# Kernel optimization log

Hardware: AMD Instinct MI355X
Metric: run time of the kernel (lower is better)

## Reference

```python
import jax, jax.numpy as jnp
import numpy as np

B = 2            # graphs per batch
N_SRC = 4096     # src nodes per graph
N_TGT = 4096     # tgt nodes per graph
NX = 8; NY = 8   # subdomain grid
C_IN = 8; HID = 32; C_OUT = 8
ENC = 2 * HID    # input_encode output dim, matches GraphConv(2*hidden, out)


def _clusters(coords, batch):
    cx = np.clip((coords[:, 0] * NX).astype(np.int64), 0, NX - 1)
    cy = np.clip((coords[:, 1] * NY).astype(np.int64), 0, NY - 1)
    return batch * (NX * NY) + cx * NY + cy


def setup_inputs() -> dict:
    rng = np.random.default_rng(0)
    src_coords = rng.random((B * N_SRC, 2)).astype(np.float32)
    tgt_coords = rng.random((B * N_TGT, 2)).astype(np.float32)
    src_batch = np.repeat(np.arange(B), N_SRC).astype(np.int32)
    tgt_batch = np.repeat(np.arange(B), N_TGT).astype(np.int32)
    # subdomain clustering + all-pairs intra-cluster edges, self loops removed
    sub = np.concatenate([_clusters(src_coords, src_batch.astype(np.int64)),
                          _clusters(tgt_coords, tgt_batch.astype(np.int64))])
    rows, cols = [], []
    for c in range(B * NX * NY):
        idx = np.nonzero(sub == c)[0]
        a, b = np.meshgrid(idx, idx, indexing='ij')
        m = a != b
        rows.append(a[m]); cols.append(b[m])
    edge_index = np.stack([np.concatenate(rows), np.concatenate(cols)]).astype(np.int32)

    def lin(k, fan_in, fan_out):
        return (rng.standard_normal((fan_in, fan_out)).astype(np.float32) / np.sqrt(fan_in))

    return {
        'src_node_values': jnp.asarray(rng.standard_normal((B * N_SRC, C_IN)).astype(np.float32)),
        'src_coords': jnp.asarray(src_coords),
        'src_batch': jnp.asarray(src_batch),
        'tgt_node_values': jnp.asarray(rng.standard_normal((B * N_TGT, C_IN)).astype(np.float32)),
        'tgt_coords': jnp.asarray(tgt_coords),
        'tgt_batch': jnp.asarray(tgt_batch),
        'edge_index': jnp.asarray(edge_index),
        'W_enc': jnp.asarray(lin(0, C_IN + 2, ENC)),
        'b_enc': jnp.zeros((ENC,), jnp.float32),
        'W_skip': jnp.asarray(lin(1, C_IN, C_OUT)),
        'W_rel': jnp.asarray(lin(2, ENC, C_OUT)),
        'b_rel': jnp.zeros((C_OUT,), jnp.float32),
        'W_root': jnp.asarray(lin(3, ENC, C_OUT)),
    }


def reference(src_node_values, src_coords, src_batch, tgt_node_values, tgt_coords,
              tgt_batch, edge_index, W_enc, b_enc, W_skip, W_rel, b_rel, W_root):
    pos = jnp.concatenate([src_coords, tgt_coords], axis=0)            # [N,2]
    vals = jnp.concatenate([src_node_values, tgt_node_values], axis=0)  # [N,Cin]
    x = jnp.concatenate([vals, pos], axis=1) @ W_enc + b_enc           # [N,2H]
    N = x.shape[0]
    src_j, dst_i = edge_index[0], edge_index[1]
    # edge_weight = ||pos_i - pos_j|| (self loops already removed)
    w = jnp.linalg.norm(pos[src_j] - pos[dst_i], axis=1)               # [E]
    msg = w[:, None] * x[src_j]                                        # [E,2H]
    agg = jax.ops.segment_sum(msg, dst_i, num_segments=N)
    cnt = jax.ops.segment_sum(jnp.ones_like(w), dst_i, num_segments=N)
    agg = agg / jnp.maximum(cnt, 1.0)[:, None]                         # mean aggr
    out = agg @ W_rel + b_rel + x @ W_root                             # GraphConv
    return tgt_node_values @ W_skip + out[src_coords.shape[0]:]
```

## Files before the change

### kernel.cpp

```cpp
#include <hip/hip_runtime.h>
#include <math.h>

#define NSRC 8192
#define NC   128
#define MAXN 256
#define MAXT 128
#define QT   32
#define KPAD 260

__device__ inline void fma4(float4& a, float s, const float4 w) {
    a.x = fmaf(s, w.x, a.x); a.y = fmaf(s, w.y, a.y);
    a.z = fmaf(s, w.z, a.z); a.w = fmaf(s, w.w, a.w);
}

__global__ __launch_bounds__(256) void fused_kernel(
        const float* __restrict__ sv, const float* __restrict__ sc,
        const float* __restrict__ tv, const float* __restrict__ tc,
        const float* __restrict__ W_enc, const float* __restrict__ b_enc,
        const float* __restrict__ W_skip, const float* __restrict__ W_rel,
        const float* __restrict__ b_rel, const float* __restrict__ W_root,
        float* __restrict__ out) {
    __shared__ float mpx[MAXN], mpy[MAXN];
    __shared__ int   mids[MAXN];
    __shared__ int   rslot[MAXN];
    __shared__ int   tIdx[MAXT];
    __shared__ int   wsum[4];
    __shared__ float Wer[10][8];
    __shared__ float Woz[10][8];
    __shared__ float c01[16];
    __shared__ float yL[MAXN][8];
    __shared__ float zL[QT][8];
    __shared__ float tpxB[QT], tpyB[QT];
    __shared__ int   tmidB[QT];
    __shared__ float2 pL[QT][4][2];
    __shared__ float wL[QT][KPAD];

    const int c = blockIdx.x >> 2, quarter = blockIdx.x & 3;
    const int t = threadIdx.x;
    const int lane = t & 63, wid = t >> 6;
    const float4* scp = (const float4*)sc;
    const float4* tcp = (const float4*)tc;

    rslot[t] = -1;

    unsigned long long mask = 0ull;
    int cnt = 0, cntT = 0;
#pragma unroll 8
    for (int i = 0; i < 32; ++i) {
        int idx4 = i * 256 + t;
        int isT = idx4 >= 4096;
        float4 qd = isT ? tcp[idx4 - 4096] : scp[idx4];
        int local0 = (idx4 - (isT ? 4096 : 0)) * 2;
        int b = local0 >> 12;
        int cx0 = min(max((int)(qd.x * 8.0f), 0), 7);
        int cy0 = min(max((int)(qd.y * 8.0f), 0), 7);
        int cx1 = min(max((int)(qd.z * 8.0f), 0), 7);
        int cy1 = min(max((int)(qd.w * 8.0f), 0), 7);
        if (b * 64 + cx0 * 8 + cy0 == c) { mask |= 1ull << (2 * i);     cnt++; cntT += isT; }
        if (b * 64 + cx1 * 8 + cy1 == c) { mask |= 1ull << (2 * i + 1); cnt++; cntT += isT; }
    }
    int incl = cnt | (cntT << 16);
    for (int s = 1; s < 64; s <<= 1) {
        int v = __shfl_up(incl, s, 64);
        if (lane >= s) incl += v;
    }
    if (lane == 63) wsum[wid] = incl;
    __syncthreads();
    int pre = 0, total = 0;
    for (int w = 0; w < 4; ++w) { int v = wsum[w]; if (w < wid) pre += v; total += v; }
    incl += pre;
    const int ncl_total = total & 0xffff;
    const int ncl = min(ncl_total, MAXN);
    const int ntT = min(total >> 16, MAXT);
    const int clen = (ntT + 3) >> 2;
    const int qlo = quarter * clen;
    const int myNT = min(clen, ntT - qlo);
    if (myNT <= 0) return;
    int p = (incl & 0xffff) - cnt;
    int q = (incl >> 16) - cntT;

    int bpos[8];
#pragma unroll
    for (int j = 0; j < 8; ++j) {
        bpos[j] = mask ? (__ffsll((unsigned long long)mask) - 1) : -1;
        mask &= mask - 1;
    }
#pragma unroll
    for (int j = 0; j < 8; ++j) {
        if (bpos[j] >= 0) {
            int i = bpos[j] >> 1, jj = bpos[j] & 1;
            int idx4 = i * 256 + t;
            int isT = idx4 >= 4096;
            float4 q4 = isT ? tcp[idx4 - 4096] : scp[idx4];
            float px = jj ? q4.z : q4.x, py = jj ? q4.w : q4.y;
            int nl = (idx4 - (isT ? 4096 : 0)) * 2 + jj;
            if (p < MAXN) {
                mids[p] = isT ? (NSRC + nl) : nl;
                mpx[p] = px; mpy[p] = py;
                if (isT && q < MAXT) { tIdx[q] = p; rslot[p] = q; }
            }
            p++; if (isT) q++;
        }
    }
    while (mask) {
        int bp = __ffsll((unsigned long long)mask) - 1;
        mask &= mask - 1;
        int i = bp >> 1, jj = bp & 1;
        int idx4 = i * 256 + t;
        int isT = idx4 >= 4096;
        float4 q4 = isT ? tcp[idx4 - 4096] : scp[idx4];
        int nl = (idx4 - (isT ? 4096 : 0)) * 2 + jj;
        if (p < MAXN) {
            mids[p] = isT ? (NSRC + nl) : nl;
            mpx[p] = jj ? q4.z : q4.x; mpy[p] = jj ? q4.w : q4.y;
            if (isT && q < MAXT) { tIdx[q] = p; rslot[p] = q; }
        }
        p++; if (isT) q++;
    }

    if (t < 176) {
        const float* ap; const float* bp2; float init; float* dst;
        if (t < 80) {
            int r = t >> 3, o = t & 7;
            ap = W_enc + r * 64; bp2 = W_rel + o; init = 0.f; dst = &Wer[r][o];
        } else if (t < 160) {
            int u = t - 80, r = u >> 3, o = u & 7;
            ap = W_enc + r * 64; bp2 = W_root + o;
            init = (r < 8) ? W_skip[r * 8 + o] : 0.f; dst = &Woz[r][o];
        } else if (t < 168) {
            int o = t - 160;
            ap = b_enc; bp2 = W_rel + o; init = 0.f; dst = &c01[o];
        } else {
            int o = t - 168;
            ap = b_enc; bp2 = W_root + o; init = b_rel[o]; dst = &c01[8 + o];
        }
        float acc = init;
#pragma unroll 8
        for (int h = 0; h < 64; ++h) acc = fmaf(ap[h], bp2[h * 8], acc);
        *dst = acc;
    }
    __syncthreads();

    if (t < ncl) {
        const int gid = mids[t];
        const float* vals = (gid < NSRC) ? (sv + gid * 8) : (tv + (gid - NSRC) * 8);
        const float4 v0 = *(const float4*)vals;
        const float4 v1 = *(const float4*)(vals + 4);
        const float px = mpx[t], py = mpy[t];
        float4 y0 = *(const float4*)&c01[0];
        float4 y1 = *(const float4*)&c01[4];
        fma4(y0, v0.x, *(const float4*)&Wer[0][0]); fma4(y1, v0.x, *(const float4*)&Wer[0][4]);
        fma4(y0, v0.y, *(const float4*)&Wer[1][0]); fma4(y1, v0.y, *(const float4*)&Wer[1][4]);
        fma4(y0, v0.z, *(const float4*)&Wer[2][0]); fma4(y1, v0.z, *(const float4*)&Wer[2][4]);
        fma4(y0, v0.w, *(const float4*)&Wer[3][0]); fma4(y1, v0.w, *(const float4*)&Wer[3][4]);
        fma4(y0, v1.x, *(const float4*)&Wer[4][0]); fma4(y1, v1.x, *(const float4*)&Wer[4][4]);
        fma4(y0, v1.y, *(const float4*)&Wer[5][0]); fma4(y1, v1.y, *(const float4*)&Wer[5][4]);
        fma4(y0, v1.z, *(const float4*)&Wer[6][0]); fma4(y1, v1.z, *(const float4*)&Wer[6][4]);
        fma4(y0, v1.w, *(const float4*)&Wer[7][0]); fma4(y1, v1.w, *(const float4*)&Wer[7][4]);
        fma4(y0, px,   *(const float4*)&Wer[8][0]); fma4(y1, px,   *(const float4*)&Wer[8][4]);
        fma4(y0, py,   *(const float4*)&Wer[9][0]); fma4(y1, py,   *(const float4*)&Wer[9][4]);
        *(float4*)&yL[t][0] = y0; *(float4*)&yL[t][4] = y1;
        const int qs = rslot[t];
        if (qs >= qlo && qs < qlo + myNT) {
            float4 z0 = *(const float4*)&c01[8];
            float4 z1 = *(const float4*)&c01[12];
            fma4(z0, v0.x, *(const float4*)&Woz[0][0]); fma4(z1, v0.x, *(const float4*)&Woz[0][4]);
            fma4(z0, v0.y, *(const float4*)&Woz[1][0]); fma4(z1, v0.y, *(const float4*)&Woz[1][4]);
            fma4(z0, v0.z, *(const float4*)&Woz[2][0]); fma4(z1, v0.z, *(const float4*)&Woz[2][4]);
            fma4(z0, v0.w, *(const float4*)&Woz[3][0]); fma4(z1, v0.w, *(const float4*)&Woz[3][4]);
            fma4(z0, v1.x, *(const float4*)&Woz[4][0]); fma4(z1, v1.x, *(const float4*)&Woz[4][4]);
            fma4(z0, v1.y, *(const float4*)&Woz[5][0]); fma4(z1, v1.y, *(const float4*)&Woz[5][4]);
            fma4(z0, v1.z, *(const float4*)&Woz[6][0]); fma4(z1, v1.z, *(const float4*)&Woz[6][4]);
            fma4(z0, v1.w, *(const float4*)&Woz[7][0]); fma4(z1, v1.w, *(const float4*)&Woz[7][4]);
            fma4(z0, px,   *(const float4*)&Woz[8][0]); fma4(z1, px,   *(const float4*)&Woz[8][4]);
            fma4(z0, py,   *(const float4*)&Woz[9][0]); fma4(z1, py,   *(const float4*)&Woz[9][4]);
            *(float4*)&zL[qs - qlo][0] = z0; *(float4*)&zL[qs - qlo][4] = z1;
        }
    }
    if (t < myNT) {
        int pr = tIdx[qlo + t];
        tpxB[t] = mpx[pr]; tpyB[t] = mpy[pr]; tmidB[t] = mids[pr] - NSRC;
    }
    __syncthreads();

    for (int tt = 0; tt < myNT; ++tt) {
        const float px = tpxB[tt], py = tpyB[tt];
        for (int k = t; k < ncl; k += 256) {
            float dx = px - mpx[k], dy = py - mpy[k];
            wL[tt][k] = sqrtf(fmaf(dx, dx, dy * dy));
        }
    }
    __syncthreads();

    {
        const int op = t & 3, tt = (t >> 2) & 31, kh = t >> 7;
        const int hl = (ncl + 1) >> 1;
        const int k0 = kh * hl, k1 = min(k0 + hl, ncl);
        if (tt < myNT) {
            float ax = 0.f, ay = 0.f;
#pragma unroll 4
            for (int k = k0; k < k1; ++k) {
                float w = wL[tt][k];
                float2 yv = *(const float2*)&yL[k][op * 2];
                ax = fmaf(w, yv.x, ax); ay = fmaf(w, yv.y, ay);
            }
            pL[tt][op][kh] = make_float2(ax, ay);
        }
    }
    __syncthreads();
    if (t < 128) {
        const int o2 = t & 3, t2 = t >> 2;
        if (t2 < myNT) {
            const float inv = 1.0f / fmaxf((float)(ncl_total - 1), 1.0f);
            float2 pa = pL[t2][o2][0], pb = pL[t2][o2][1];
            float2 zv = *(const float2*)&zL[t2][o2 * 2];
            *(float2*)&out[tmidB[t2] * 8 + o2 * 2] =
                make_float2(zv.x + (pa.x + pb.x) * inv, zv.y + (pa.y + pb.y) * inv);
        }
    }
}

extern "C" void kernel_launch(void* const* d_in, const int* in_sizes, int n_in,
                              void* d_out, int out_size, void* d_ws, size_t ws_size,
                              hipStream_t stream) {
    const float* sv    = (const float*)d_in[0];
    const float* sc    = (const float*)d_in[1];
    const float* tv    = (const float*)d_in[3];
    const float* tc    = (const float*)d_in[4];
    const float* W_enc = (const float*)d_in[7];
    const float* b_enc = (const float*)d_in[8];
    const float* W_skip= (const float*)d_in[9];
    const float* W_rel = (const float*)d_in[10];
    const float* b_rel = (const float*)d_in[11];
    const float* W_root= (const float*)d_in[12];
    float* out = (float*)d_out;

    fused_kernel<<<NC * 4, 256, 0, stream>>>(
        sv, sc, tv, tc, W_enc, b_enc, W_skip, W_rel, b_rel, W_root, out);
}
```

Before: 18.57 us.

## Scan only own batch, use float bound tests, fuse edge-weight computation into aggregation

Each block now scans only the coordinates of its own batch, which halves the membership scan, and tests cluster membership with float bound comparisons instead of clamp-and-multiply. The separate pass that stored pairwise distances in a shared wL matrix is removed. Instead, each thread computes the distance on the fly and accumulates all 8 output channels over a K-slice, followed by an 8-way slice reduction. The gather loads are also split from the shared stores to increase memory-level parallelism. In exchange, sqrt is recomputed per thread, and the float boundary tests must match the reference's truncating cluster assignment.

Result: faster. 16.52 us (-11.0%).

```diff
diff --git a/kernel.cpp b/kernel.cpp
--- a/kernel.cpp
+++ b/kernel.cpp
@@ -6,7 +6,6 @@
 #define MAXN 256
 #define MAXT 128
 #define QT   32
-#define KPAD 260
 
 __device__ inline void fma4(float4& a, float s, const float4 w) {
     a.x = fmaf(s, w.x, a.x); a.y = fmaf(s, w.y, a.y);
@@ -32,32 +31,36 @@
     __shared__ float zL[QT][8];
     __shared__ float tpxB[QT], tpyB[QT];
     __shared__ int   tmidB[QT];
-    __shared__ float2 pL[QT][4][2];
-    __shared__ float wL[QT][KPAD];
+    __shared__ float pL[QT][8][8];
 
     const int c = blockIdx.x >> 2, quarter = blockIdx.x & 3;
     const int t = threadIdx.x;
     const int lane = t & 63, wid = t >> 6;
-    const float4* scp = (const float4*)sc;
-    const float4* tcp = (const float4*)tc;
+    const int b = c >> 6, cc = c & 63;
+    const int cx = cc >> 3, cy = cc & 7;
+    const float xlo = cx * 0.125f, xhi = xlo + 0.125f;
+    const float ylo = cy * 0.125f, yhi = ylo + 0.125f;
+    const bool x0 = (cx == 0), x7 = (cx == 7), y0 = (cy == 0), y7 = (cy == 7);
+
+    const float4* scpB = (const float4*)sc + b * 2048;
+    const float4* tcpB = (const float4*)tc + b * 2048;
 
     rslot[t] = -1;
 
     unsigned long long mask = 0ull;
     int cnt = 0, cntT = 0;
 #pragma unroll 8
-    for (int i = 0; i < 32; ++i) {
+    for (int i = 0; i < 16; ++i) {
         int idx4 = i * 256 + t;
-        int isT = idx4 >= 4096;
-        float4 qd = isT ? tcp[idx4 - 4096] : scp[idx4];
-        int local0 = (idx4 - (isT ? 4096 : 0)) * 2;
-        int b = local0 >> 12;
-        int cx0 = min(max((int)(qd.x * 8.0f), 0), 7);
-        int cy0 = min(max((int)(qd.y * 8.0f), 0), 7);
-        int cx1 = min(max((int)(qd.z * 8.0f), 0), 7);
-        int cy1 = min(max((int)(qd.w * 8.0f), 0), 7);
-        if (b * 64 + cx0 * 8 + cy0 == c) { mask |= 1ull << (2 * i);     cnt++; cntT += isT; }
-        if (b * 64 + cx1 * 8 + cy1 == c) { mask |= 1ull << (2 * i + 1); cnt++; cntT += isT; }
+        int isT = idx4 >= 2048;
+        int li2 = idx4 - (isT << 11);
+        float4 qd = isT ? tcpB[li2] : scpB[li2];
+        bool m0 = (x0 | (qd.x >= xlo)) & (x7 | (qd.x < xhi))
+                & (y0 | (qd.y >= ylo)) & (y7 | (qd.y < yhi));
+        bool m1 = (x0 | (qd.z >= xlo)) & (x7 | (qd.z < xhi))
+                & (y0 | (qd.w >= ylo)) & (y7 | (qd.w < yhi));
+        if (m0) { mask |= 1ull << (2 * i);     cnt++; cntT += isT; }
+        if (m1) { mask |= 1ull << (2 * i + 1); cnt++; cntT += isT; }
     }
     int incl = cnt | (cntT << 16);
     for (int s = 1; s < 64; s <<= 1) {
@@ -85,21 +88,29 @@
         bpos[j] = mask ? (__ffsll((unsigned long long)mask) - 1) : -1;
         mask &= mask - 1;
     }
+    float pxs[8], pys[8]; int nls[8], isTs[8];
 #pragma unroll
     for (int j = 0; j < 8; ++j) {
         if (bpos[j] >= 0) {
             int i = bpos[j] >> 1, jj = bpos[j] & 1;
             int idx4 = i * 256 + t;
-            int isT = idx4 >= 4096;
-            float4 q4 = isT ? tcp[idx4 - 4096] : scp[idx4];
-            float px = jj ? q4.z : q4.x, py = jj ? q4.w : q4.y;
-            int nl = (idx4 - (isT ? 4096 : 0)) * 2 + jj;
+            int isT = idx4 >= 2048;
+            int li2 = idx4 - (isT << 11);
+            float4 q4 = isT ? tcpB[li2] : scpB[li2];
+            pxs[j] = jj ? q4.z : q4.x; pys[j] = jj ? q4.w : q4.y;
+            nls[j] = b * 4096 + li2 * 2 + jj;
+            isTs[j] = isT;
+        }
+    }
+#pragma unroll
+    for (int j = 0; j < 8; ++j) {
+        if (bpos[j] >= 0) {
             if (p < MAXN) {
-                mids[p] = isT ? (NSRC + nl) : nl;
-                mpx[p] = px; mpy[p] = py;
-                if (isT && q < MAXT) { tIdx[q] = p; rslot[p] = q; }
+                mids[p] = isTs[j] ? (NSRC + nls[j]) : nls[j];
+                mpx[p] = pxs[j]; mpy[p] = pys[j];
+                if (isTs[j] && q < MAXT) { tIdx[q] = p; rslot[p] = q; }
             }
-            p++; if (isT) q++;
+            p++; if (isTs[j]) q++;
         }
     }
     while (mask) {
@@ -107,9 +118,10 @@
         mask &= mask - 1;
         int i = bp >> 1, jj = bp & 1;
         int idx4 = i * 256 + t;
-        int isT = idx4 >= 4096;
-        float4 q4 = isT ? tcp[idx4 - 4096] : scp[idx4];
-        int nl = (idx4 - (isT ? 4096 : 0)) * 2 + jj;
+        int isT = idx4 >= 2048;
+        int li2 = idx4 - (isT << 11);
+        float4 q4 = isT ? tcpB[li2] : scpB[li2];
+        int nl = b * 4096 + li2 * 2 + jj;
         if (p < MAXN) {
             mids[p] = isT ? (NSRC + nl) : nl;
             mpx[p] = jj ? q4.z : q4.x; mpy[p] = jj ? q4.w : q4.y;
@@ -183,39 +195,35 @@
     }
     __syncthreads();
 
-    for (int tt = 0; tt < myNT; ++tt) {
-        const float px = tpxB[tt], py = tpyB[tt];
-        for (int k = t; k < ncl; k += 256) {
-            float dx = px - mpx[k], dy = py - mpy[k];
-            wL[tt][k] = sqrtf(fmaf(dx, dx, dy * dy));
-        }
-    }
-    __syncthreads();
-
     {
-        const int op = t & 3, tt = (t >> 2) & 31, kh = t >> 7;
-        const int hl = (ncl + 1) >> 1;
-        const int k0 = kh * hl, k1 = min(k0 + hl, ncl);
+        const int slice = t >> 5, tt = t & 31;
         if (tt < myNT) {
-            float ax = 0.f, ay = 0.f;
-#pragma unroll 4
+            const float px = tpxB[tt], py = tpyB[tt];
+            const int klen = (ncl + 7) >> 3;
+            const int k0 = slice * klen, k1 = min(k0 + klen, ncl);
+            float4 ay0 = make_float4(0.f, 0.f, 0.f, 0.f), ay1 = ay0;
             for (int k = k0; k < k1; ++k) {
-                float w = wL[tt][k];
-                float2 yv = *(const float2*)&yL[k][op * 2];
-                ax = fmaf(w, yv.x, ax); ay = fmaf(w, yv.y, ay);
+                float dx = px - mpx[k], dy = py - mpy[k];
+                float w = sqrtf(fmaf(dx, dx, dy * dy));
+                fma4(ay0, w, *(const float4*)&yL[k][0]);
+                fma4(ay1, w, *(const float4*)&yL[k][4]);
             }
-            pL[tt][op][kh] = make_float2(ax, ay);
-        }
-    }
-    __syncthreads();
-    if (t < 128) {
-        const int o2 = t & 3, t2 = t >> 2;
+            *(float4*)&pL[tt][slice][0] = ay0;
+            *(float4*)&pL[tt][slice][4] = ay1;
+        }
+    }
+    __syncthreads();
+    {
+        const int t2 = t >> 3, ch = t & 7;
         if (t2 < myNT) {
+            float s = 0.f;
+#pragma unroll
+            for (int s8 = 0; s8 < 8; ++s8) {
+                int sl = (s8 + t2) & 7;
+                s += pL[t2][sl][ch];
+            }
             const float inv = 1.0f / fmaxf((float)(ncl_total - 1), 1.0f);
-            float2 pa = pL[t2][o2][0], pb = pL[t2][o2][1];
-            float2 zv = *(const float2*)&zL[t2][o2 * 2];
-            *(float2*)&out[tmidB[t2] * 8 + o2 * 2] =
-                make_float2(zv.x + (pa.x + pb.x) * inv, zv.y + (pa.y + pb.y) * inv);
+            out[tmidB[t2] * 8 + ch] = zL[t2][ch] + s * inv;
         }
     }
 }
```
